# Kernel tuning notes

Measured on AMD Instinct MI355X. Metric: run time of the kernel, lower is better.

Reference implementation:

```python
import jax, jax.numpy as jnp
import numpy as np
from jax import lax

D_MODEL, D_STATE, D_CONV, EXPAND = 1024, 64, 4, 2
D_INNER = EXPAND * D_MODEL  # 2048
BATCH, SEQ = 4, 4096


def setup_inputs() -> dict:
    key = jax.random.key(0)
    ks = jax.random.split(key, 9)
    s = lambda fan_in: 1.0 / np.sqrt(fan_in)
    inp = {
        "x": jax.random.normal(ks[0], (BATCH, SEQ, D_MODEL), dtype=jnp.float32),
        # nn.Linear(d_model, expand*d_model + d_model, bias=False)
        "in_proj_w": jax.random.uniform(ks[1], (D_INNER + D_MODEL, D_MODEL), jnp.float32, -s(D_MODEL), s(D_MODEL)),
        # depthwise Conv1d(d_inner, d_inner, k=d_conv, groups=d_inner)
        "conv_w": jax.random.uniform(ks[2], (D_INNER, 1, D_CONV), jnp.float32, -s(D_CONV), s(D_CONV)),
        "conv_b": jax.random.uniform(ks[3], (D_INNER,), jnp.float32, -s(D_CONV), s(D_CONV)),
        # nn.Linear(d_inner, 2*d_state, bias=False)  (output unused downstream)
        "x_proj_w": jax.random.uniform(ks[4], (2 * D_STATE, D_INNER), jnp.float32, -s(D_INNER), s(D_INNER)),
        # nn.Linear(d_inner, d_inner, bias=True)
        "dt_proj_w": jax.random.uniform(ks[5], (D_INNER, D_INNER), jnp.float32, -s(D_INNER), s(D_INNER)),
        "dt_proj_b": jax.random.uniform(ks[6], (D_INNER,), jnp.float32, -s(D_INNER), s(D_INNER)),
        "A_log": jnp.log(jnp.tile(jnp.arange(1, D_STATE + 1, dtype=jnp.float32), (D_INNER, 1))),
        "D": jnp.ones((D_INNER,), dtype=jnp.float32),
        "out_proj_w": jax.random.uniform(ks[7], (D_MODEL, D_INNER), jnp.float32, -s(D_INNER), s(D_INNER)),
    }
    return inp


def _forward(x, in_proj_w, conv_w, conv_b, x_proj_w, dt_proj_w, dt_proj_b, A_log, D, out_proj_w):
    b, seq_len, d_model = x.shape
    d_inner = conv_w.shape[0]
    d_conv = conv_w.shape[-1]

    # in_proj and split into ssm path / residual path
    x_and_res = jnp.einsum("bsd,od->bso", x, in_proj_w)
    u, res = x_and_res[..., :d_inner], x_and_res[..., d_inner:]

    # causal depthwise conv1d (torch pads both sides by d_conv-1 then slices [:seq_len],
    # equivalent to left-pad only)
    u_c = lax.conv_general_dilated(
        u.transpose(0, 2, 1), conv_w, window_strides=(1,),
        padding=[(d_conv - 1, 0)], feature_group_count=d_inner,
        dimension_numbers=("NCH", "OIH", "NCH"),
    ) + conv_b[None, :, None]
    u = u_c.transpose(0, 2, 1)  # [b, s, d_inner]

    # x_proj / A / D are computed in the original module but never used by the scan.
    x_dbl = jnp.einsum("bsd,od->bso", u, x_proj_w)  # dead (delta is overwritten)
    _ = -jnp.exp(A_log)  # dead
    _ = D  # dead

    # delta = softplus(dt_proj(u)); scan gate
    delta = jax.nn.softplus(jnp.einsum("bsd,od->bso", u, dt_proj_w) + dt_proj_b)
    gated_u = u * jax.nn.sigmoid(delta)

    # EMA recurrence: state = 0.9*state + 0.1*gated_u[t]
    def step(state, u_t):
        state = state * 0.9 + u_t * 0.1
        return state, state

    _, ys = lax.scan(step, jnp.zeros((b, d_inner), dtype=u.dtype), gated_u.transpose(1, 0, 2))
    y = ys.transpose(1, 0, 2)  # [b, s, d_inner]

    return jnp.einsum("bsd,od->bso", y, out_proj_w) + res


def reference(x, in_proj_w, conv_w, conv_b, x_proj_w, dt_proj_w, dt_proj_b, A_log, D, out_proj_w):
    return _forward(x, in_proj_w, conv_w, conv_b, x_proj_w, dt_proj_w, dt_proj_b, A_log, D, out_proj_w)
```

## Files before the change

kernel.cpp:

```cpp
#include <hip/hip_runtime.h>
#include <stdint.h>
#include <math.h>

#define D_MODEL 1024
#define D_INNER 2048
#define N_RES   1024
#define SEQ     4096
#define BATCH   4
#define M_TOT   (BATCH*SEQ)
#define SMEM_BYTES 131072

typedef float f32x4 __attribute__((ext_vector_type(4)));
typedef float f32x16 __attribute__((ext_vector_type(16)));
typedef short bf16x8 __attribute__((ext_vector_type(8)));
typedef int   i32x4v __attribute__((ext_vector_type(4)));
typedef int   i32x8  __attribute__((ext_vector_type(8)));
typedef unsigned short u16;
typedef unsigned char u8;

__device__ __forceinline__ u16 f2bf(float f) {
  uint32_t u = __builtin_bit_cast(uint32_t, f);
  u += 0x7FFFu + ((u >> 16) & 1u);
  return (u16)(u >> 16);
}
__device__ __forceinline__ float bf2f(u16 h) {
  return __builtin_bit_cast(float, (uint32_t)h << 16);
}

__device__ __forceinline__ uint32_t enc1_e4m3(float f) {
  uint32_t b = __builtin_bit_cast(uint32_t, f);
  uint32_t s = (b >> 24) & 0x80u;
  uint32_t a = b & 0x7FFFFFFFu;
  if (a >= 0x43E00000u) return s | 0x7Eu;
  if (a < 0x3C800000u) {
    float q = __builtin_bit_cast(float, a) * 512.f;
    uint32_t m = (uint32_t)(q + 0.5f);
    return s | (m > 7u ? 8u : m);
  }
  uint32_t lsb = (a >> 20) & 1u;
  a += 0x0007FFFFu + lsb;
  uint32_t e8 = (a >> 23) - 120u;
  if (e8 >= 16u) return s | 0x7Eu;
  return s | (e8 << 3) | ((a >> 20) & 7u);
}
__device__ __forceinline__ float dec1_e4m3(uint32_t v) {
  uint32_t e = (v >> 3) & 15u, m = v & 7u;
  float mag = e ? __builtin_bit_cast(float, ((e + 120u) << 23) | (m << 20))
                : (float)m * 0.001953125f;
  return (v & 0x80u) ? -mag : mag;
}
template<bool HI>
__device__ __forceinline__ int pk_fp8(float a, float b, int old) {
#if __has_builtin(__builtin_amdgcn_cvt_pk_fp8_f32)
  return __builtin_amdgcn_cvt_pk_fp8_f32(a, b, old, HI);
#else
  uint32_t w = enc1_e4m3(a) | (enc1_e4m3(b) << 8);
  return HI ? (int)(((uint32_t)old & 0xFFFFu) | (w << 16))
            : (int)(((uint32_t)old & 0xFFFF0000u) | w);
#endif
}
template<int SEL>
__device__ __forceinline__ float up_fp8(int w) {
#if __has_builtin(__builtin_amdgcn_cvt_f32_fp8)
  return __builtin_amdgcn_cvt_f32_fp8(w, SEL);
#else
  return dec1_e4m3(((uint32_t)w >> (SEL * 8)) & 0xFFu);
#endif
}

__device__ __forceinline__ void g2l16(const void* g, void* l) {
  __builtin_amdgcn_global_load_lds(
      (const __attribute__((address_space(1))) void*)g,
      (__attribute__((address_space(3))) void*)l, 16, 0, 0);
}

#define CVT_N0 4194304
#define CVT_N1  786432
#define CVT_N2 1048576
#define CVT_N3  524288
#define CVT_TOT (CVT_N0+CVT_N1+CVT_N2+CVT_N3)

__global__ void cvt_all_kernel(const float* __restrict__ s0, u16* __restrict__ d0,
                               const float* __restrict__ s1, u16* __restrict__ d1,
                               const float* __restrict__ s2, u8* __restrict__ d2,
                               const float* __restrict__ s3, u8* __restrict__ d3) {
  const int stride = gridDim.x * blockDim.x;
  for (int i = blockIdx.x * blockDim.x + threadIdx.x; i < CVT_TOT; i += stride) {
    int j = i;
    if (j < CVT_N0 + CVT_N1) {
      const float* src; u16* dst;
      if (j < CVT_N0) { src = s0; dst = d0; } else { j -= CVT_N0; src = s1; dst = d1; }
      f32x4 v = *(const f32x4*)(src + (size_t)j * 4);
      ushort4 o;
      o.x = f2bf(v.x); o.y = f2bf(v.y); o.z = f2bf(v.z); o.w = f2bf(v.w);
      *(ushort4*)(dst + (size_t)j * 4) = o;
    } else {
      j -= CVT_N0 + CVT_N1;
      const float* src; u8* dst;
      if (j < CVT_N2) { src = s2; dst = d2; } else { j -= CVT_N2; src = s3; dst = d3; }
      f32x4 v = *(const f32x4*)(src + (size_t)j * 4);
      int p = 0;
      p = pk_fp8<false>(v.x * 16.f, v.y * 16.f, p);
      p = pk_fp8<true >(v.z * 16.f, v.w * 16.f, p);
      *(int*)(dst + (size_t)j * 4) = p;
    }
  }
}

template<int EPI, int K, int NBX>
__global__ __launch_bounds__(512, 2) void gemm256(
    const u16* __restrict__ A, const u16* __restrict__ B,
    void* __restrict__ out0, void* __restrict__ out1,
    const float* __restrict__ bias)
{
  extern __shared__ char smem[];
  constexpr int NT = K / 32;
  const int tid  = threadIdx.x;
  const int lane = tid & 63;
  const int wave = tid >> 6;
  const int wm = wave >> 2, wn = wave & 3;

  const int nb  = (M_TOT / 256) * NBX;
  const int cpx = nb >> 3;
  const int wg  = ((int)blockIdx.x & 7) * cpx + ((int)blockIdx.x >> 3);
  const int m0 = (wg / NBX) << 8;
  const int n0 = (wg % NBX) << 8;

  const int st_row = (wave << 4) + (lane >> 2);
  const int st_kc  = (((lane & 3) ^ ((lane >> 3) & 3)) << 3);
  const u16* pA0 = A + (size_t)(m0 + st_row) * K + st_kc;
  const u16* pA1 = pA0 + (size_t)128 * K;
  const u16* pB0 = B + (size_t)(n0 + st_row) * K + st_kc;
  const u16* pB1 = pB0 + (size_t)128 * K;
  const int st_lds = wave << 10;

  const int l15 = lane & 15, k16 = lane >> 4;
  const int chunk = ((k16 ^ ((l15 >> 1) & 3)) << 4);
  const int aoff = (((wm << 7) + l15) << 6) + chunk;
  const int boff = (((wn << 6) + l15) << 6) + chunk;

  f32x4 acc[8][4] = {};
  bf16x8 fa0[8], fb0[4], fa1[8], fb1[4];

#define STAGE(ts_) do {                                   \
    char* ab_ = smem + (((ts_) & 3) << 14);               \
    char* bb_ = smem + 65536 + (((ts_) & 3) << 14);       \
    const int kt_ = (ts_) << 5;                           \
    g2l16(pA0 + kt_, ab_ + st_lds);                       \
    g2l16(pA1 + kt_, ab_ + 8192 + st_lds);                \
    g2l16(pB0 + kt_, bb_ + st_lds);                       \
    g2l16(pB1 + kt_, bb_ + 8192 + st_lds);                \
  } while (0)

#define READF(tr_, RA_, RB_) do {                                   \
    const char* Ab_ = smem + (((tr_) & 3) << 14);                   \
    const char* Bb_ = smem + 65536 + (((tr_) & 3) << 14);           \
    _Pragma("unroll")                                               \
    for (int i_ = 0; i_ < 8; ++i_)                                  \
      RA_[i_] = *(const bf16x8*)(Ab_ + aoff + (i_ << 10));          \
    _Pragma("unroll")                                               \
    for (int j_ = 0; j_ < 4; ++j_)                                  \
      RB_[j_] = *(const bf16x8*)(Bb_ + boff + (j_ << 10));          \
  } while (0)

#define ONE_ITER(t_, RA_, RB_, MA_, MB_) do {                        \
    if ((t_) + 1 < NT) {                                             \
      if ((t_) + 2 < NT) asm volatile("s_waitcnt vmcnt(4)" ::: "memory"); \
      else               asm volatile("s_waitcnt vmcnt(0)" ::: "memory"); \
      __builtin_amdgcn_s_barrier();                                  \
      __builtin_amdgcn_sched_barrier(0);                             \
      READF((t_) + 1, RA_, RB_);                                     \
    }                                                                \
    if ((t_) + 3 < NT) STAGE((t_) + 3);                              \
    __builtin_amdgcn_sched_barrier(0);                               \
    __builtin_amdgcn_s_setprio(1);                                   \
    _Pragma("unroll")                                                \
    for (int j_ = 0; j_ < 4; ++j_) {                                 \
      _Pragma("unroll")                                              \
      for (int i_ = 0; i_ < 8; ++i_)                                 \
        acc[i_][j_] = __builtin_amdgcn_mfma_f32_16x16x32_bf16(MA_[i_], MB_[j_], acc[i_][j_], 0, 0, 0); \
    }                                                                \
    __builtin_amdgcn_s_setprio(0);                                   \
    __builtin_amdgcn_sched_barrier(0);                               \
  } while (0)

  #pragma unroll
  for (int pt = 0; pt < 3; ++pt) STAGE(pt);
  asm volatile("s_waitcnt vmcnt(8)" ::: "memory");
  __builtin_amdgcn_s_barrier();
  __builtin_amdgcn_sched_barrier(0);
  READF(0, fa0, fb0);

  for (int t = 0; t < NT; t += 2) {
    ONE_ITER(t,     fa1, fb1, fa0, fb0);
    ONE_ITER(t + 1, fa0, fb0, fa1, fb1);
  }
#undef STAGE
#undef READF
#undef ONE_ITER

  __syncthreads();
  float (*sc)[260] = (float(*)[260])smem;
  const int lr = (lane >> 4) << 2;
  const int lc = lane & 15;
  #pragma unroll
  for (int p = 0; p < 4; ++p) {
    if (wm == (p >> 1)) {
      const int ib = (p & 1) << 2;
      #pragma unroll
      for (int ii = 0; ii < 4; ++ii)
        #pragma unroll
        for (int j = 0; j < 4; ++j)
          #pragma unroll
          for (int r = 0; r < 4; ++r)
            sc[(ii << 4) + lr + r][(wn << 6) + (j << 4) + lc] = acc[ib + ii][j][r];
    }
    __syncthreads();
    #pragma unroll
    for (int rr = 0; rr < 8; ++rr) {
      const int row = (rr << 3) + wave;
      const int col = (tid & 63) << 2;
      const f32x4 v = *(const f32x4*)&sc[row][col];
      const int gr = m0 + (p << 6) + row;
      const int gc = n0 + col;
      ushort4 o;
      o.x = f2bf(v.x); o.y = f2bf(v.y); o.z = f2bf(v.z); o.w = f2bf(v.w);
      if (n0 < D_INNER)
        *(ushort4*)&((u16*)out0)[(size_t)gr * D_INNER + gc] = o;
      else
        *(ushort4*)&((u16*)out1)[(size_t)gr * N_RES + (gc - D_INNER)] = o;
    }
    __syncthreads();
  }
}

template<int EPI, int K, int NBX>
__global__ __launch_bounds__(512, 2) void gemm256mx(
    const u8* __restrict__ A, const u8* __restrict__ B,
    void* __restrict__ out0, void* __restrict__ out1,
    const float* __restrict__ bias)
{
  extern __shared__ char smem[];
  constexpr int NT = K / 64;
  const int tid  = threadIdx.x;
  const int lane = tid & 63;
  const int wave = tid >> 6;
  const int wm = wave >> 2, wn = wave & 3;

  const int nb  = (M_TOT / 256) * NBX;
  const int cpx = nb >> 3;
  const int wg  = ((int)blockIdx.x & 7) * cpx + ((int)blockIdx.x >> 3);
  const int m0 = (wg / NBX) << 8;
  const int n0 = (wg % NBX) << 8;

  const int st_row = (wave << 4) + (lane >> 2);
  const int st_kc  = (((lane & 3) ^ ((lane >> 3) & 3)) << 4);
  const u8* pA0 = A + (size_t)(m0 + st_row) * K + st_kc;
  const u8* pA1 = pA0 + (size_t)128 * K;
  const u8* pB0 = B + (size_t)(n0 + st_row) * K + st_kc;
  const u8* pB1 = pB0 + (size_t)128 * K;
  const int st_lds = wave << 10;

  const int l31 = lane & 31;
  const int x2  = (l31 >> 1) & 3;
  const int c0  = (lane >> 5) << 1;
  const int slot0 = ((c0     ^ x2) << 4);
  const int slot1 = (((c0+1) ^ x2) << 4);
  const int abase = ((wm << 7) + l31) << 6;
  const int bbase = ((wn << 6) + l31) << 6;

  f32x16 acc[4][2] = {};
  i32x8 fa[4], fb[2];

#define STAGE(ts_) do {                                   \
    char* ab_ = smem + (((ts_) & 3) << 14);               \
    char* bb_ = smem + 65536 + (((ts_) & 3) << 14);       \
    const int kt_ = (ts_) << 6;                           \
    g2l16(pA0 + kt_, ab_ + st_lds);                       \
    g2l16(pA1 + kt_, ab_ + 8192 + st_lds);                \
    g2l16(pB0 + kt_, bb_ + st_lds);                       \
    g2l16(pB1 + kt_, bb_ + 8192 + st_lds);                \
  } while (0)

#define READF(tr_) do {                                               \
    const char* Ab_ = smem + (((tr_) & 3) << 14);                     \
    const char* Bb_ = smem + 65536 + (((tr_) & 3) << 14);             \
    _Pragma("unroll")                                                 \
    for (int i_ = 0; i_ < 4; ++i_) {                                  \
      const char* p_ = Ab_ + abase + (i_ << 11);                      \
      i32x4v lo_ = *(const i32x4v*)(p_ + slot0);                      \
      i32x4v hi_ = *(const i32x4v*)(p_ + slot1);                      \
      i32x8 v_;                                                       \
      v_[0]=lo_[0]; v_[1]=lo_[1]; v_[2]=lo_[2]; v_[3]=lo_[3];         \
      v_[4]=hi_[0]; v_[5]=hi_[1]; v_[6]=hi_[2]; v_[7]=hi_[3];         \
      fa[i_] = v_;                                                    \
    }                                                                 \
    _Pragma("unroll")                                                 \
    for (int j_ = 0; j_ < 2; ++j_) {                                  \
      const char* p_ = Bb_ + bbase + (j_ << 11);                      \
      i32x4v lo_ = *(const i32x4v*)(p_ + slot0);                      \
      i32x4v hi_ = *(const i32x4v*)(p_ + slot1);                      \
      i32x8 v_;                                                       \
      v_[0]=lo_[0]; v_[1]=lo_[1]; v_[2]=lo_[2]; v_[3]=lo_[3];         \
      v_[4]=hi_[0]; v_[5]=hi_[1]; v_[6]=hi_[2]; v_[7]=hi_[3];         \
      fb[j_] = v_;                                                    \
    }                                                                 \
  } while (0)

  #pragma unroll
  for (int pt = 0; pt < 3; ++pt) STAGE(pt);

  for (int t = 0; t < NT; ++t) {
    if (t + 2 < NT)      asm volatile("s_waitcnt vmcnt(8)" ::: "memory");
    else if (t + 1 < NT) asm volatile("s_waitcnt vmcnt(4)" ::: "memory");
    else                 asm volatile("s_waitcnt vmcnt(0)" ::: "memory");
    __builtin_amdgcn_s_barrier();
    __builtin_amdgcn_sched_barrier(0);
    READF(t);
    if (t + 3 < NT) STAGE(t + 3);
    __builtin_amdgcn_sched_barrier(0);
    __builtin_amdgcn_s_setprio(1);
    #pragma unroll
    for (int j_ = 0; j_ < 2; ++j_) {
      #pragma unroll
      for (int i_ = 0; i_ < 4; ++i_)
        acc[i_][j_] = __builtin_amdgcn_mfma_scale_f32_32x32x64_f8f6f4(
            fa[i_], fb[j_], acc[i_][j_], 0, 0,
            0, 0x7F7F7F7F, 0, 0x7F7F7F7F);
    }
    __builtin_amdgcn_s_setprio(0);
    __builtin_amdgcn_sched_barrier(0);
  }
#undef STAGE
#undef READF

  __syncthreads();
  float (*sc)[260] = (float(*)[260])smem;
  const int r32b = ((lane >> 5) << 2);
  #pragma unroll
  for (int p = 0; p < 4; ++p) {
    if (wm == (p >> 1)) {
      #pragma unroll
      for (int it = 0; it < 2; ++it) {
        const int i_ = ((p & 1) << 1) + it;
        #pragma unroll
        for (int j = 0; j < 2; ++j)
          #pragma unroll
          for (int r = 0; r < 16; ++r) {
            const int r32 = (r & 3) + ((r >> 2) << 3) + r32b;
            sc[(it << 5) + r32][(wn << 6) + (j << 5) + l31] = acc[i_][j][r];
          }
      }
    }
    __syncthreads();
    #pragma unroll
    for (int rr = 0; rr < 8; ++rr) {
      const int row = (rr << 3) + wave;
      const int col = (tid & 63) << 2;
      const f32x4 v = *(const f32x4*)&sc[row][col];
      const int gr = m0 + (p << 6) + row;
      const int gc = n0 + col;
      if constexpr (EPI == 1) {
        const f32x4 b4 = *(const f32x4*)&bias[gc];
        const int uw = *(const int*)&((const u8*)out1)[(size_t)gr * D_INNER + gc];
        const float ucv[4] = { up_fp8<0>(uw), up_fp8<1>(uw), up_fp8<2>(uw), up_fp8<3>(uw) };
        float vv[4] = {v.x, v.y, v.z, v.w};
        float bb[4] = {b4.x, b4.y, b4.z, b4.w};
        u16   oo[4];
        #pragma unroll
        for (int q = 0; q < 4; ++q) {
          const float d  = vv[q] * 0.0009765625f + bb[q];
          const float sp = (d > 15.f) ? d : __logf(1.f + __expf(d));
          const float sg = 1.f / (1.f + __expf(-sp));
          oo[q] = f2bf(ucv[q] * 0.015625f * sg);
        }
        ushort4 o; o.x = oo[0]; o.y = oo[1]; o.z = oo[2]; o.w = oo[3];
        *(ushort4*)&((u16*)out0)[(size_t)gr * D_INNER + gc] = o;
      } else {
        const ushort4 rv = *(const ushort4*)&((const u16*)out1)[(size_t)gr * N_RES + gc];
        f32x4 o;
        o.x = v.x * 0.0009765625f + bf2f(rv.x);
        o.y = v.y * 0.0009765625f + bf2f(rv.y);
        o.z = v.z * 0.0009765625f + bf2f(rv.z);
        o.w = v.w * 0.0009765625f + bf2f(rv.w);
        *(f32x4*)&((float*)out0)[(size_t)gr * N_RES + gc] = o;
      }
    }
    __syncthreads();
  }
}

__global__ __launch_bounds__(256) void conv_kernel(
    const u16* __restrict__ u, u8* __restrict__ uc,
    const float* __restrict__ cw, const float* __restrict__ cb)
{
  const int c0 = threadIdx.x * 8;
  const int b  = blockIdx.x >> 8;
  const int t0 = (blockIdx.x & 255) << 4;
  const size_t base = (size_t)b * SEQ * D_INNER;

  float w0[8], w1[8], w2[8], w3[8], bs[8];
  #pragma unroll
  for (int j = 0; j < 8; ++j) {
    const float* wp = cw + (size_t)(c0 + j) * 4;
    w0[j] = wp[0]; w1[j] = wp[1]; w2[j] = wp[2]; w3[j] = wp[3];
    bs[j] = cb[c0 + j];
  }

  float r0[8], r1[8], r2[8];
  #pragma unroll
  for (int k = 0; k < 3; ++k) {
    const int t = t0 - 3 + k;
    float* rr = (k == 0) ? r0 : (k == 1) ? r1 : r2;
    if (t >= 0) {
      bf16x8 v = *(const bf16x8*)&u[base + (size_t)t * D_INNER + c0];
      #pragma unroll
      for (int j = 0; j < 8; ++j) rr[j] = bf2f((u16)v[j]);
    } else {
      #pragma unroll
      for (int j = 0; j < 8; ++j) rr[j] = 0.f;
    }
  }

  #pragma unroll
  for (int tt = 0; tt < 16; ++tt) {
    const size_t off = base + (size_t)(t0 + tt) * D_INNER + c0;
    bf16x8 v = *(const bf16x8*)&u[off];
    float cur[8], s[8];
    #pragma unroll
    for (int j = 0; j < 8; ++j) cur[j] = bf2f((u16)v[j]);
    #pragma unroll
    for (int j = 0; j < 8; ++j)
      s[j] = (bs[j] + w0[j]*r0[j] + w1[j]*r1[j] + w2[j]*r2[j] + w3[j]*cur[j]) * 64.f;
    int p0 = 0, p1 = 0;
    p0 = pk_fp8<false>(s[0], s[1], p0); p0 = pk_fp8<true>(s[2], s[3], p0);
    p1 = pk_fp8<false>(s[4], s[5], p1); p1 = pk_fp8<true>(s[6], s[7], p1);
    int2 o; o.x = p0; o.y = p1;
    *(int2*)&uc[off] = o;
    #pragma unroll
    for (int j = 0; j < 8; ++j) { r0[j] = r1[j]; r1[j] = r2[j]; r2[j] = cur[j]; }
  }
}

__global__ __launch_bounds__(256) void scan_kernel(const u16* __restrict__ g, u8* __restrict__ y) {
  const int cg    = blockIdx.x & 1;
  const int chunk = (blockIdx.x >> 1) & 31;
  const int b     = blockIdx.x >> 6;
  const int c0 = cg * 1024 + threadIdx.x * 4;
  const int t0 = chunk << 7;
  const size_t base = (size_t)b * SEQ * D_INNER + c0;
  float s0 = 0.f, s1 = 0.f, s2 = 0.f, s3 = 0.f;
  const int tw = (t0 >= 96) ? t0 - 96 : 0;
  for (int t = tw; t < t0; ++t) {
    ushort4 v = *(const ushort4*)&g[base + (size_t)t * D_INNER];
    s0 = s0*0.9f + bf2f(v.x)*0.1f; s1 = s1*0.9f + bf2f(v.y)*0.1f;
    s2 = s2*0.9f + bf2f(v.z)*0.1f; s3 = s3*0.9f + bf2f(v.w)*0.1f;
  }
  for (int t = t0; t < t0 + 128; ++t) {
    ushort4 v = *(const ushort4*)&g[base + (size_t)t * D_INNER];
    s0 = s0*0.9f + bf2f(v.x)*0.1f; s1 = s1*0.9f + bf2f(v.y)*0.1f;
    s2 = s2*0.9f + bf2f(v.z)*0.1f; s3 = s3*0.9f + bf2f(v.w)*0.1f;
    int p = 0;
    p = pk_fp8<false>(s0 * 64.f, s1 * 64.f, p);
    p = pk_fp8<true >(s2 * 64.f, s3 * 64.f, p);
    *(int*)&y[base + (size_t)t * D_INNER] = p;
  }
}

extern "C" void kernel_launch(void* const* d_in, const int* in_sizes, int n_in,
                              void* d_out, int out_size, void* d_ws, size_t ws_size,
                              hipStream_t stream) {
  (void)in_sizes; (void)n_in; (void)out_size; (void)ws_size;
  const float* x  = (const float*)d_in[0];
  const float* w1 = (const float*)d_in[1];
  const float* cw = (const float*)d_in[2];
  const float* cb = (const float*)d_in[3];
  const float* w2 = (const float*)d_in[5];
  const float* db = (const float*)d_in[6];
  const float* w3 = (const float*)d_in[9];

  char* ws = (char*)d_ws;
  u16* x_bf   = (u16*)(ws);
  u16* w1_bf  = (u16*)(ws + 33554432);
  u8*  w2_f8  = (u8*) (ws + 39845888);
  u8*  w3_f8  = (u8*) (ws + 44040192);
  u16* u_bf   = (u16*)(ws + 46137344);
  u16* res_bf = (u16*)(ws + 113246208);
  u8*  uc_f8  = (u8*) (ws + 146800640);
  u8*  y_f8   = (u8*) (ws + 180355072);

  (void)hipFuncSetAttribute((const void*)&gemm256<0,1024,12>,   hipFuncAttributeMaxDynamicSharedMemorySize, SMEM_BYTES);
  (void)hipFuncSetAttribute((const void*)&gemm256mx<1,2048,8>,  hipFuncAttributeMaxDynamicSharedMemorySize, SMEM_BYTES);
  (void)hipFuncSetAttribute((const void*)&gemm256mx<2,2048,4>,  hipFuncAttributeMaxDynamicSharedMemorySize, SMEM_BYTES);

  cvt_all_kernel<<<2048, 256, 0, stream>>>(x, x_bf, w1, w1_bf, w2, w2_f8, w3, w3_f8);

  gemm256<0, 1024, 12><<<768, 512, SMEM_BYTES, stream>>>(x_bf, w1_bf, u_bf, res_bf, nullptr);
  conv_kernel<<<1024, 256, 0, stream>>>(u_bf, uc_f8, cw, cb);
  gemm256mx<1, 2048, 8><<<512, 512, SMEM_BYTES, stream>>>(uc_f8, w2_f8, u_bf, uc_f8, db);
  scan_kernel<<<256, 256, 0, stream>>>(u_bf, y_f8);
  gemm256mx<2, 2048, 4><<<256, 512, SMEM_BYTES, stream>>>(y_f8, w3_f8, d_out, res_bf, nullptr);
}
```

Before: 328.9 us.

## Move u-projection to FP8 GEMM and store intermediates as FP8

Splits the in_proj GEMM in two. The u half (2048 outputs) now runs on the FP8 MX GEMM path with FP8 output, and the residual half stays bf16. Conv and scan inputs and the gated intermediate are now stored as FP8 instead of bf16, which halves their memory traffic, and the scale factors are folded into the new layouts. The conversion kernel now also produces an FP8 copy of x. This lowers GEMM compute cost and bandwidth but adds an extra read of x and more quantization error in the u path.

```diff
diff --git a/kernel.cpp b/kernel.cpp
--- a/kernel.cpp
+++ b/kernel.cpp
@@ -75,43 +75,62 @@
 }
 
 #define CVT_N0 4194304
-#define CVT_N1  786432
-#define CVT_N2 1048576
-#define CVT_N3  524288
-#define CVT_TOT (CVT_N0+CVT_N1+CVT_N2+CVT_N3)
-
-__global__ void cvt_all_kernel(const float* __restrict__ s0, u16* __restrict__ d0,
-                               const float* __restrict__ s1, u16* __restrict__ d1,
-                               const float* __restrict__ s2, u8* __restrict__ d2,
-                               const float* __restrict__ s3, u8* __restrict__ d3) {
+#define CVT_N1  524288
+#define CVT_N2  262144
+#define CVT_N3 1048576
+#define CVT_N4  524288
+#define CVT_TOT (CVT_N0+CVT_N1+CVT_N2+CVT_N3+CVT_N4)
+
+__global__ void cvt_all_kernel(const float* __restrict__ x,  u16* __restrict__ x_bf,
+                               u8* __restrict__ x_f8,
+                               const float* __restrict__ w1, u8* __restrict__ w1u_f8,
+                               u16* __restrict__ w1r_bf,
+                               const float* __restrict__ w2, u8* __restrict__ w2_f8,
+                               const float* __restrict__ w3, u8* __restrict__ w3_f8) {
   const int stride = gridDim.x * blockDim.x;
   for (int i = blockIdx.x * blockDim.x + threadIdx.x; i < CVT_TOT; i += stride) {
     int j = i;
-    if (j < CVT_N0 + CVT_N1) {
-      const float* src; u16* dst;
-      if (j < CVT_N0) { src = s0; dst = d0; } else { j -= CVT_N0; src = s1; dst = d1; }
-      f32x4 v = *(const f32x4*)(src + (size_t)j * 4);
+    if (j < CVT_N0) {
+      f32x4 v = *(const f32x4*)(x + (size_t)j * 4);
       ushort4 o;
       o.x = f2bf(v.x); o.y = f2bf(v.y); o.z = f2bf(v.z); o.w = f2bf(v.w);
-      *(ushort4*)(dst + (size_t)j * 4) = o;
-    } else {
-      j -= CVT_N0 + CVT_N1;
-      const float* src; u8* dst;
-      if (j < CVT_N2) { src = s2; dst = d2; } else { j -= CVT_N2; src = s3; dst = d3; }
-      f32x4 v = *(const f32x4*)(src + (size_t)j * 4);
+      *(ushort4*)(x_bf + (size_t)j * 4) = o;
       int p = 0;
       p = pk_fp8<false>(v.x * 16.f, v.y * 16.f, p);
       p = pk_fp8<true >(v.z * 16.f, v.w * 16.f, p);
-      *(int*)(dst + (size_t)j * 4) = p;
-    }
-  }
-}
-
-template<int EPI, int K, int NBX>
-__global__ __launch_bounds__(512, 2) void gemm256(
+      *(int*)(x_f8 + (size_t)j * 4) = p;
+    } else if ((j -= CVT_N0) < CVT_N1) {
+      f32x4 v = *(const f32x4*)(w1 + (size_t)j * 4);
+      int p = 0;
+      p = pk_fp8<false>(v.x * 16.f, v.y * 16.f, p);
+      p = pk_fp8<true >(v.z * 16.f, v.w * 16.f, p);
+      *(int*)(w1u_f8 + (size_t)j * 4) = p;
+    } else if ((j -= CVT_N1) < CVT_N2) {
+      f32x4 v = *(const f32x4*)(w1 + (size_t)(D_INNER * D_MODEL / 4 + j) * 4);
+      ushort4 o;
+      o.x = f2bf(v.x); o.y = f2bf(v.y); o.z = f2bf(v.z); o.w = f2bf(v.w);
+      *(ushort4*)(w1r_bf + (size_t)j * 4) = o;
+    } else if ((j -= CVT_N2) < CVT_N3) {
+      f32x4 v = *(const f32x4*)(w2 + (size_t)j * 4);
+      int p = 0;
+      p = pk_fp8<false>(v.x * 16.f, v.y * 16.f, p);
+      p = pk_fp8<true >(v.z * 16.f, v.w * 16.f, p);
+      *(int*)(w2_f8 + (size_t)j * 4) = p;
+    } else {
+      j -= CVT_N3;
+      f32x4 v = *(const f32x4*)(w3 + (size_t)j * 4);
+      int p = 0;
+      p = pk_fp8<false>(v.x * 16.f, v.y * 16.f, p);
+      p = pk_fp8<true >(v.z * 16.f, v.w * 16.f, p);
+      *(int*)(w3_f8 + (size_t)j * 4) = p;
+    }
+  }
+}
+
+template<int K, int NBX>
+__global__ __launch_bounds__(512, 2) void gemm256res(
     const u16* __restrict__ A, const u16* __restrict__ B,
-    void* __restrict__ out0, void* __restrict__ out1,
-    const float* __restrict__ bias)
+    u16* __restrict__ out0)
 {
   extern __shared__ char smem[];
   constexpr int NT = K / 32;
@@ -225,10 +244,7 @@
       const int gc = n0 + col;
       ushort4 o;
       o.x = f2bf(v.x); o.y = f2bf(v.y); o.z = f2bf(v.z); o.w = f2bf(v.w);
-      if (n0 < D_INNER)
-        *(ushort4*)&((u16*)out0)[(size_t)gr * D_INNER + gc] = o;
-      else
-        *(ushort4*)&((u16*)out1)[(size_t)gr * N_RES + (gc - D_INNER)] = o;
+      *(ushort4*)&out0[(size_t)gr * N_RES + gc] = o;
     }
     __syncthreads();
   }
@@ -360,22 +376,29 @@
       const f32x4 v = *(const f32x4*)&sc[row][col];
       const int gr = m0 + (p << 6) + row;
       const int gc = n0 + col;
-      if constexpr (EPI == 1) {
+      if constexpr (EPI == 0) {
+        int pk = 0;
+        pk = pk_fp8<false>(v.x * 0.25f, v.y * 0.25f, pk);
+        pk = pk_fp8<true >(v.z * 0.25f, v.w * 0.25f, pk);
+        *(int*)&((u8*)out0)[(size_t)gr * D_INNER + gc] = pk;
+      } else if constexpr (EPI == 1) {
         const f32x4 b4 = *(const f32x4*)&bias[gc];
         const int uw = *(const int*)&((const u8*)out1)[(size_t)gr * D_INNER + gc];
-        const float ucv[4] = { up_fp8<0>(uw), up_fp8<1>(uw), up_fp8<2>(uw), up_fp8<3>(uw) };
+        const float ucr[4] = { up_fp8<0>(uw), up_fp8<1>(uw), up_fp8<2>(uw), up_fp8<3>(uw) };
         float vv[4] = {v.x, v.y, v.z, v.w};
         float bb[4] = {b4.x, b4.y, b4.z, b4.w};
-        u16   oo[4];
+        float gg[4];
         #pragma unroll
         for (int q = 0; q < 4; ++q) {
           const float d  = vv[q] * 0.0009765625f + bb[q];
           const float sp = (d > 15.f) ? d : __logf(1.f + __expf(d));
           const float sg = 1.f / (1.f + __expf(-sp));
-          oo[q] = f2bf(ucv[q] * 0.015625f * sg);
+          gg[q] = ucr[q] * sg;
         }
-        ushort4 o; o.x = oo[0]; o.y = oo[1]; o.z = oo[2]; o.w = oo[3];
-        *(ushort4*)&((u16*)out0)[(size_t)gr * D_INNER + gc] = o;
+        int pk = 0;
+        pk = pk_fp8<false>(gg[0], gg[1], pk);
+        pk = pk_fp8<true >(gg[2], gg[3], pk);
+        *(int*)&((u8*)out0)[(size_t)gr * D_INNER + gc] = pk;
       } else {
         const ushort4 rv = *(const ushort4*)&((const u16*)out1)[(size_t)gr * N_RES + gc];
         f32x4 o;
@@ -391,7 +414,7 @@
 }
 
 __global__ __launch_bounds__(256) void conv_kernel(
-    const u16* __restrict__ u, u8* __restrict__ uc,
+    const u8* __restrict__ u, u8* __restrict__ uc,
     const float* __restrict__ cw, const float* __restrict__ cb)
 {
   const int c0 = threadIdx.x * 8;
@@ -404,7 +427,7 @@
   for (int j = 0; j < 8; ++j) {
     const float* wp = cw + (size_t)(c0 + j) * 4;
     w0[j] = wp[0]; w1[j] = wp[1]; w2[j] = wp[2]; w3[j] = wp[3];
-    bs[j] = cb[c0 + j];
+    bs[j] = cb[c0 + j] * 64.f;
   }
 
   float r0[8], r1[8], r2[8];
@@ -413,9 +436,11 @@
     const int t = t0 - 3 + k;
     float* rr = (k == 0) ? r0 : (k == 1) ? r1 : r2;
     if (t >= 0) {
-      bf16x8 v = *(const bf16x8*)&u[base + (size_t)t * D_INNER + c0];
-      #pragma unroll
-      for (int j = 0; j < 8; ++j) rr[j] = bf2f((u16)v[j]);
+      int2 v = *(const int2*)&u[base + (size_t)t * D_INNER + c0];
+      rr[0] = up_fp8<0>(v.x); rr[1] = up_fp8<1>(v.x);
+      rr[2] = up_fp8<2>(v.x); rr[3] = up_fp8<3>(v.x);
+      rr[4] = up_fp8<0>(v.y); rr[5] = up_fp8<1>(v.y);
+      rr[6] = up_fp8<2>(v.y); rr[7] = up_fp8<3>(v.y);
     } else {
       #pragma unroll
       for (int j = 0; j < 8; ++j) rr[j] = 0.f;
@@ -425,13 +450,15 @@
   #pragma unroll
   for (int tt = 0; tt < 16; ++tt) {
     const size_t off = base + (size_t)(t0 + tt) * D_INNER + c0;
-    bf16x8 v = *(const bf16x8*)&u[off];
+    int2 v = *(const int2*)&u[off];
     float cur[8], s[8];
-    #pragma unroll
-    for (int j = 0; j < 8; ++j) cur[j] = bf2f((u16)v[j]);
+    cur[0] = up_fp8<0>(v.x); cur[1] = up_fp8<1>(v.x);
+    cur[2] = up_fp8<2>(v.x); cur[3] = up_fp8<3>(v.x);
+    cur[4] = up_fp8<0>(v.y); cur[5] = up_fp8<1>(v.y);
+    cur[6] = up_fp8<2>(v.y); cur[7] = up_fp8<3>(v.y);
     #pragma unroll
     for (int j = 0; j < 8; ++j)
-      s[j] = (bs[j] + w0[j]*r0[j] + w1[j]*r1[j] + w2[j]*r2[j] + w3[j]*cur[j]) * 64.f;
+      s[j] = bs[j] + w0[j]*r0[j] + w1[j]*r1[j] + w2[j]*r2[j] + w3[j]*cur[j];
     int p0 = 0, p1 = 0;
     p0 = pk_fp8<false>(s[0], s[1], p0); p0 = pk_fp8<true>(s[2], s[3], p0);
     p1 = pk_fp8<false>(s[4], s[5], p1); p1 = pk_fp8<true>(s[6], s[7], p1);
@@ -442,7 +469,7 @@
   }
 }
 
-__global__ __launch_bounds__(256) void scan_kernel(const u16* __restrict__ g, u8* __restrict__ y) {
+__global__ __launch_bounds__(256) void scan_kernel(const u8* __restrict__ g, u8* __restrict__ y) {
   const int cg    = blockIdx.x & 1;
   const int chunk = (blockIdx.x >> 1) & 31;
   const int b     = blockIdx.x >> 6;
@@ -452,17 +479,17 @@
   float s0 = 0.f, s1 = 0.f, s2 = 0.f, s3 = 0.f;
   const int tw = (t0 >= 96) ? t0 - 96 : 0;
   for (int t = tw; t < t0; ++t) {
-    ushort4 v = *(const ushort4*)&g[base + (size_t)t * D_INNER];
-    s0 = s0*0.9f + bf2f(v.x)*0.1f; s1 = s1*0.9f + bf2f(v.y)*0.1f;
-    s2 = s2*0.9f + bf2f(v.z)*0.1f; s3 = s3*0.9f + bf2f(v.w)*0.1f;
+    const int v = *(const int*)&g[base + (size_t)t * D_INNER];
+    s0 = s0*0.9f + up_fp8<0>(v)*0.1f; s1 = s1*0.9f + up_fp8<1>(v)*0.1f;
+    s2 = s2*0.9f + up_fp8<2>(v)*0.1f; s3 = s3*0.9f + up_fp8<3>(v)*0.1f;
   }
   for (int t = t0; t < t0 + 128; ++t) {
-    ushort4 v = *(const ushort4*)&g[base + (size_t)t * D_INNER];
-    s0 = s0*0.9f + bf2f(v.x)*0.1f; s1 = s1*0.9f + bf2f(v.y)*0.1f;
-    s2 = s2*0.9f + bf2f(v.z)*0.1f; s3 = s3*0.9f + bf2f(v.w)*0.1f;
+    const int v = *(const int*)&g[base + (size_t)t * D_INNER];
+    s0 = s0*0.9f + up_fp8<0>(v)*0.1f; s1 = s1*0.9f + up_fp8<1>(v)*0.1f;
+    s2 = s2*0.9f + up_fp8<2>(v)*0.1f; s3 = s3*0.9f + up_fp8<3>(v)*0.1f;
     int p = 0;
-    p = pk_fp8<false>(s0 * 64.f, s1 * 64.f, p);
-    p = pk_fp8<true >(s2 * 64.f, s3 * 64.f, p);
+    p = pk_fp8<false>(s0, s1, p);
+    p = pk_fp8<true >(s2, s3, p);
     *(int*)&y[base + (size_t)t * D_INNER] = p;
   }
 }
@@ -480,24 +507,30 @@
   const float* w3 = (const float*)d_in[9];
 
   char* ws = (char*)d_ws;
-  u16* x_bf   = (u16*)(ws);
-  u16* w1_bf  = (u16*)(ws + 33554432);
-  u8*  w2_f8  = (u8*) (ws + 39845888);
-  u8*  w3_f8  = (u8*) (ws + 44040192);
-  u16* u_bf   = (u16*)(ws + 46137344);
-  u16* res_bf = (u16*)(ws + 113246208);
-  u8*  uc_f8  = (u8*) (ws + 146800640);
-  u8*  y_f8   = (u8*) (ws + 180355072);
-
-  (void)hipFuncSetAttribute((const void*)&gemm256<0,1024,12>,   hipFuncAttributeMaxDynamicSharedMemorySize, SMEM_BYTES);
+  u16* x_bf    = (u16*)(ws);
+  u8*  x_f8    = (u8*) (ws + 33554432);
+  u8*  w1u_f8  = (u8*) (ws + 50331648);
+  u16* w1r_bf  = (u16*)(ws + 52428800);
+  u8*  w2_f8   = (u8*) (ws + 54525952);
+  u8*  w3_f8   = (u8*) (ws + 58720256);
+  u8*  u_f8    = (u8*) (ws + 60817408);
+  u16* res_bf  = (u16*)(ws + 94371840);
+  u8*  uc_f8   = (u8*) (ws + 127926272);
+  u8*  gated_f8 = (u8*)(ws);
+  u8*  y_f8    = u_f8;
+
+  (void)hipFuncSetAttribute((const void*)&gemm256res<1024,4>,   hipFuncAttributeMaxDynamicSharedMemorySize, SMEM_BYTES);
+  (void)hipFuncSetAttribute((const void*)&gemm256mx<0,1024,8>,  hipFuncAttributeMaxDynamicSharedMemorySize, SMEM_BYTES);
   (void)hipFuncSetAttribute((const void*)&gemm256mx<1,2048,8>,  hipFuncAttributeMaxDynamicSharedMemorySize, SMEM_BYTES);
   (void)hipFuncSetAttribute((const void*)&gemm256mx<2,2048,4>,  hipFuncAttributeMaxDynamicSharedMemorySize, SMEM_BYTES);
 
-  cvt_all_kernel<<<2048, 256, 0, stream>>>(x, x_bf, w1, w1_bf, w2, w2_f8, w3, w3_f8);
-
-  gemm256<0, 1024, 12><<<768, 512, SMEM_BYTES, stream>>>(x_bf, w1_bf, u_bf, res_bf, nullptr);
-  conv_kernel<<<1024, 256, 0, stream>>>(u_bf, uc_f8, cw, cb);
-  gemm256mx<1, 2048, 8><<<512, 512, SMEM_BYTES, stream>>>(uc_f8, w2_f8, u_bf, uc_f8, db);
-  scan_kernel<<<256, 256, 0, stream>>>(u_bf, y_f8);
+  cvt_all_kernel<<<2048, 256, 0, stream>>>(x, x_bf, x_f8, w1, w1u_f8, w1r_bf,
+                                           w2, w2_f8, w3, w3_f8);
+
+  gemm256mx<0, 1024, 8><<<512, 512, SMEM_BYTES, stream>>>(x_f8, w1u_f8, u_f8, nullptr, nullptr);
+  gemm256res<1024, 4><<<256, 512, SMEM_BYTES, stream>>>(x_bf, w1r_bf, res_bf);
+  conv_kernel<<<1024, 256, 0, stream>>>(u_f8, uc_f8, cw, cb);
+  gemm256mx<1, 2048, 8><<<512, 512, SMEM_BYTES, stream>>>(uc_f8, w2_f8, gated_f8, uc_f8, db);
+  scan_kernel<<<256, 256, 0, stream>>>(gated_f8, y_f8);
   gemm256mx<2, 2048, 4><<<256, 512, SMEM_BYTES, stream>>>(y_f8, w3_f8, d_out, res_bf, nullptr);
 }
```

Result: no change. 335.4 us (+2.0%).

## Store u and gated intermediates as fp8 instead of bf16

Applied to the files above, without the earlier changes.

The in_proj output u and the gated scan input are now stored as scaled fp8 instead of bf16, and the conv and scan kernels read fp8. The scale factors are folded so that u is kept at 64x scale through the conv and gate. This halves the intermediate traffic through global memory across three kernels. It costs precision in the conv input and the scan input, since fp8 rounding errors accumulate.

```diff
diff --git a/kernel.cpp b/kernel.cpp
--- a/kernel.cpp
+++ b/kernel.cpp
@@ -107,11 +107,10 @@
   }
 }
 
-template<int EPI, int K, int NBX>
-__global__ __launch_bounds__(512, 2) void gemm256(
+template<int K, int NBX>
+__global__ __launch_bounds__(512, 2) void gemm256bf(
     const u16* __restrict__ A, const u16* __restrict__ B,
-    void* __restrict__ out0, void* __restrict__ out1,
-    const float* __restrict__ bias)
+    u8* __restrict__ out_u, u16* __restrict__ out_res)
 {
   extern __shared__ char smem[];
   constexpr int NT = K / 32;
@@ -223,12 +222,16 @@
       const f32x4 v = *(const f32x4*)&sc[row][col];
       const int gr = m0 + (p << 6) + row;
       const int gc = n0 + col;
-      ushort4 o;
-      o.x = f2bf(v.x); o.y = f2bf(v.y); o.z = f2bf(v.z); o.w = f2bf(v.w);
-      if (n0 < D_INNER)
-        *(ushort4*)&((u16*)out0)[(size_t)gr * D_INNER + gc] = o;
-      else
-        *(ushort4*)&((u16*)out1)[(size_t)gr * N_RES + (gc - D_INNER)] = o;
+      if (n0 < D_INNER) {
+        int pk = 0;
+        pk = pk_fp8<false>(v.x * 64.f, v.y * 64.f, pk);
+        pk = pk_fp8<true >(v.z * 64.f, v.w * 64.f, pk);
+        *(int*)&out_u[(size_t)gr * D_INNER + gc] = pk;
+      } else {
+        ushort4 o;
+        o.x = f2bf(v.x); o.y = f2bf(v.y); o.z = f2bf(v.z); o.w = f2bf(v.w);
+        *(ushort4*)&out_res[(size_t)gr * N_RES + (gc - D_INNER)] = o;
+      }
     }
     __syncthreads();
   }
@@ -363,19 +366,21 @@
       if constexpr (EPI == 1) {
         const f32x4 b4 = *(const f32x4*)&bias[gc];
         const int uw = *(const int*)&((const u8*)out1)[(size_t)gr * D_INNER + gc];
-        const float ucv[4] = { up_fp8<0>(uw), up_fp8<1>(uw), up_fp8<2>(uw), up_fp8<3>(uw) };
+        const float ucr[4] = { up_fp8<0>(uw), up_fp8<1>(uw), up_fp8<2>(uw), up_fp8<3>(uw) };
         float vv[4] = {v.x, v.y, v.z, v.w};
         float bb[4] = {b4.x, b4.y, b4.z, b4.w};
-        u16   oo[4];
+        float gg[4];
         #pragma unroll
         for (int q = 0; q < 4; ++q) {
           const float d  = vv[q] * 0.0009765625f + bb[q];
           const float sp = (d > 15.f) ? d : __logf(1.f + __expf(d));
           const float sg = 1.f / (1.f + __expf(-sp));
-          oo[q] = f2bf(ucv[q] * 0.015625f * sg);
+          gg[q] = ucr[q] * sg;
         }
-        ushort4 o; o.x = oo[0]; o.y = oo[1]; o.z = oo[2]; o.w = oo[3];
-        *(ushort4*)&((u16*)out0)[(size_t)gr * D_INNER + gc] = o;
+        int pk = 0;
+        pk = pk_fp8<false>(gg[0], gg[1], pk);
+        pk = pk_fp8<true >(gg[2], gg[3], pk);
+        *(int*)&((u8*)out0)[(size_t)gr * D_INNER + gc] = pk;
       } else {
         const ushort4 rv = *(const ushort4*)&((const u16*)out1)[(size_t)gr * N_RES + gc];
         f32x4 o;
@@ -391,7 +396,7 @@
 }
 
 __global__ __launch_bounds__(256) void conv_kernel(
-    const u16* __restrict__ u, u8* __restrict__ uc,
+    const u8* __restrict__ u, u8* __restrict__ uc,
     const float* __restrict__ cw, const float* __restrict__ cb)
 {
   const int c0 = threadIdx.x * 8;
@@ -404,7 +409,7 @@
   for (int j = 0; j < 8; ++j) {
     const float* wp = cw + (size_t)(c0 + j) * 4;
     w0[j] = wp[0]; w1[j] = wp[1]; w2[j] = wp[2]; w3[j] = wp[3];
-    bs[j] = cb[c0 + j];
+    bs[j] = cb[c0 + j] * 64.f;
   }
 
   float r0[8], r1[8], r2[8];
@@ -413,9 +418,11 @@
     const int t = t0 - 3 + k;
     float* rr = (k == 0) ? r0 : (k == 1) ? r1 : r2;
     if (t >= 0) {
-      bf16x8 v = *(const bf16x8*)&u[base + (size_t)t * D_INNER + c0];
-      #pragma unroll
-      for (int j = 0; j < 8; ++j) rr[j] = bf2f((u16)v[j]);
+      int2 v = *(const int2*)&u[base + (size_t)t * D_INNER + c0];
+      rr[0] = up_fp8<0>(v.x); rr[1] = up_fp8<1>(v.x);
+      rr[2] = up_fp8<2>(v.x); rr[3] = up_fp8<3>(v.x);
+      rr[4] = up_fp8<0>(v.y); rr[5] = up_fp8<1>(v.y);
+      rr[6] = up_fp8<2>(v.y); rr[7] = up_fp8<3>(v.y);
     } else {
       #pragma unroll
       for (int j = 0; j < 8; ++j) rr[j] = 0.f;
@@ -425,13 +432,15 @@
   #pragma unroll
   for (int tt = 0; tt < 16; ++tt) {
     const size_t off = base + (size_t)(t0 + tt) * D_INNER + c0;
-    bf16x8 v = *(const bf16x8*)&u[off];
+    int2 v = *(const int2*)&u[off];
     float cur[8], s[8];
-    #pragma unroll
-    for (int j = 0; j < 8; ++j) cur[j] = bf2f((u16)v[j]);
+    cur[0] = up_fp8<0>(v.x); cur[1] = up_fp8<1>(v.x);
+    cur[2] = up_fp8<2>(v.x); cur[3] = up_fp8<3>(v.x);
+    cur[4] = up_fp8<0>(v.y); cur[5] = up_fp8<1>(v.y);
+    cur[6] = up_fp8<2>(v.y); cur[7] = up_fp8<3>(v.y);
     #pragma unroll
     for (int j = 0; j < 8; ++j)
-      s[j] = (bs[j] + w0[j]*r0[j] + w1[j]*r1[j] + w2[j]*r2[j] + w3[j]*cur[j]) * 64.f;
+      s[j] = bs[j] + w0[j]*r0[j] + w1[j]*r1[j] + w2[j]*r2[j] + w3[j]*cur[j];
     int p0 = 0, p1 = 0;
     p0 = pk_fp8<false>(s[0], s[1], p0); p0 = pk_fp8<true>(s[2], s[3], p0);
     p1 = pk_fp8<false>(s[4], s[5], p1); p1 = pk_fp8<true>(s[6], s[7], p1);
@@ -442,7 +451,7 @@
   }
 }
 
-__global__ __launch_bounds__(256) void scan_kernel(const u16* __restrict__ g, u8* __restrict__ y) {
+__global__ __launch_bounds__(256) void scan_kernel(const u8* __restrict__ g, u8* __restrict__ y) {
   const int cg    = blockIdx.x & 1;
   const int chunk = (blockIdx.x >> 1) & 31;
   const int b     = blockIdx.x >> 6;
@@ -452,17 +461,17 @@
   float s0 = 0.f, s1 = 0.f, s2 = 0.f, s3 = 0.f;
   const int tw = (t0 >= 96) ? t0 - 96 : 0;
   for (int t = tw; t < t0; ++t) {
-    ushort4 v = *(const ushort4*)&g[base + (size_t)t * D_INNER];
-    s0 = s0*0.9f + bf2f(v.x)*0.1f; s1 = s1*0.9f + bf2f(v.y)*0.1f;
-    s2 = s2*0.9f + bf2f(v.z)*0.1f; s3 = s3*0.9f + bf2f(v.w)*0.1f;
+    const int v = *(const int*)&g[base + (size_t)t * D_INNER];
+    s0 = s0*0.9f + up_fp8<0>(v)*0.1f; s1 = s1*0.9f + up_fp8<1>(v)*0.1f;
+    s2 = s2*0.9f + up_fp8<2>(v)*0.1f; s3 = s3*0.9f + up_fp8<3>(v)*0.1f;
   }
   for (int t = t0; t < t0 + 128; ++t) {
-    ushort4 v = *(const ushort4*)&g[base + (size_t)t * D_INNER];
-    s0 = s0*0.9f + bf2f(v.x)*0.1f; s1 = s1*0.9f + bf2f(v.y)*0.1f;
-    s2 = s2*0.9f + bf2f(v.z)*0.1f; s3 = s3*0.9f + bf2f(v.w)*0.1f;
+    const int v = *(const int*)&g[base + (size_t)t * D_INNER];
+    s0 = s0*0.9f + up_fp8<0>(v)*0.1f; s1 = s1*0.9f + up_fp8<1>(v)*0.1f;
+    s2 = s2*0.9f + up_fp8<2>(v)*0.1f; s3 = s3*0.9f + up_fp8<3>(v)*0.1f;
     int p = 0;
-    p = pk_fp8<false>(s0 * 64.f, s1 * 64.f, p);
-    p = pk_fp8<true >(s2 * 64.f, s3 * 64.f, p);
+    p = pk_fp8<false>(s0, s1, p);
+    p = pk_fp8<true >(s2, s3, p);
     *(int*)&y[base + (size_t)t * D_INNER] = p;
   }
 }
@@ -480,24 +489,25 @@
   const float* w3 = (const float*)d_in[9];
 
   char* ws = (char*)d_ws;
-  u16* x_bf   = (u16*)(ws);
-  u16* w1_bf  = (u16*)(ws + 33554432);
-  u8*  w2_f8  = (u8*) (ws + 39845888);
-  u8*  w3_f8  = (u8*) (ws + 44040192);
-  u16* u_bf   = (u16*)(ws + 46137344);
-  u16* res_bf = (u16*)(ws + 113246208);
-  u8*  uc_f8  = (u8*) (ws + 146800640);
-  u8*  y_f8   = (u8*) (ws + 180355072);
-
-  (void)hipFuncSetAttribute((const void*)&gemm256<0,1024,12>,   hipFuncAttributeMaxDynamicSharedMemorySize, SMEM_BYTES);
+  u16* x_bf    = (u16*)(ws);
+  u16* w1_bf   = (u16*)(ws + 33554432);
+  u8*  w2_f8   = (u8*) (ws + 39845888);
+  u8*  w3_f8   = (u8*) (ws + 44040192);
+  u8*  u_f8    = (u8*) (ws + 46137344);
+  u8*  uc_f8   = (u8*) (ws + 79691776);
+  u8*  gated_f8= (u8*) (ws + 113246208);
+  u8*  y_f8    = (u8*) (ws + 146800640);
+  u16* res_bf  = (u16*)(ws + 180355072);
+
+  (void)hipFuncSetAttribute((const void*)&gemm256bf<1024,12>,   hipFuncAttributeMaxDynamicSharedMemorySize, SMEM_BYTES);
   (void)hipFuncSetAttribute((const void*)&gemm256mx<1,2048,8>,  hipFuncAttributeMaxDynamicSharedMemorySize, SMEM_BYTES);
   (void)hipFuncSetAttribute((const void*)&gemm256mx<2,2048,4>,  hipFuncAttributeMaxDynamicSharedMemorySize, SMEM_BYTES);
 
   cvt_all_kernel<<<2048, 256, 0, stream>>>(x, x_bf, w1, w1_bf, w2, w2_f8, w3, w3_f8);
 
-  gemm256<0, 1024, 12><<<768, 512, SMEM_BYTES, stream>>>(x_bf, w1_bf, u_bf, res_bf, nullptr);
-  conv_kernel<<<1024, 256, 0, stream>>>(u_bf, uc_f8, cw, cb);
-  gemm256mx<1, 2048, 8><<<512, 512, SMEM_BYTES, stream>>>(uc_f8, w2_f8, u_bf, uc_f8, db);
-  scan_kernel<<<256, 256, 0, stream>>>(u_bf, y_f8);
+  gemm256bf<1024, 12><<<768, 512, SMEM_BYTES, stream>>>(x_bf, w1_bf, u_f8, res_bf);
+  conv_kernel<<<1024, 256, 0, stream>>>(u_f8, uc_f8, cw, cb);
+  gemm256mx<1, 2048, 8><<<512, 512, SMEM_BYTES, stream>>>(uc_f8, w2_f8, gated_f8, uc_f8, db);
+  scan_kernel<<<256, 256, 0, stream>>>(gated_f8, y_f8);
   gemm256mx<2, 2048, 4><<<256, 512, SMEM_BYTES, stream>>>(y_f8, w3_f8, d_out, res_bf, nullptr);
 }
```

Measured after the change: 314.7 us. 1.05x faster.
